# Optimization experiments

Hardware: AMD Instinct MI355X
Metric: run time of the kernel (lower is better)

Reference implementation:

```python
import jax, jax.numpy as jnp
import numpy as np

VARIANCE = 1.0  # prototorch euclidean_similarity default


def setup_inputs() -> dict:
    key = jax.random.key(0)
    k1, k2, k3 = jax.random.split(key, 3)
    B, D = 32768, 1024
    K, C = 5, 3  # sum([2,1,2]) components, len([2,1,2]) classes
    x = jax.random.normal(k1, (B, D), dtype=jnp.float32)
    components = jax.random.normal(k2, (K, D), dtype=jnp.float32)
    # PPRI: random probabilistic reasonings in [0,1], shape [K, C, 2]
    reasonings = jax.random.uniform(k3, (K, C, 2), dtype=jnp.float32)
    return {"x": x, "components": components, "reasonings": reasonings}


def reference(x, components, reasonings):
    # --- euclidean similarity: exp(-d(x, c)^2 / (2*variance)) ---
    # squared pairwise distances via expansion (avoids [B,K,D] intermediate)
    x2 = jnp.sum(x * x, axis=-1, keepdims=True)          # [B,1]
    c2 = jnp.sum(components * components, axis=-1)       # [K]
    d2 = x2 + c2[None, :] - 2.0 * (x @ components.T)     # [B,K]
    d2 = jnp.maximum(d2, 0.0)
    sims = jnp.exp(-d2 / (2.0 * VARIANCE))               # [B,K]

    # --- cbcc competition ---
    # reasonings [K,C,2] -> permute(2,1,0) -> [2,C,K], clamp to [0,1]
    R = jnp.clip(jnp.transpose(reasonings, (2, 1, 0)), 0.0, 1.0)
    A, Bneg = R[0], R[1]                                 # each [C,K]
    pk = A
    nk = (1.0 - A) * Bneg                                # [C,K]
    numerator = sims @ (pk - nk).T + jnp.sum(nk, axis=1) # [B,C]
    probs = numerator / jnp.sum(pk + nk, axis=1)         # [B,C]
    return probs
```

## Files before the change

kernel.cpp:

```cpp
#include <hip/hip_runtime.h>


#define DD 1024
#define KK 5
#define CC 3
#define F4_PER_ROW (DD / 4)
#define F4_PER_LANE (F4_PER_ROW / 64)

__global__ __launch_bounds__(256) void cbc_kernel(
    const float* __restrict__ x,
    const float* __restrict__ comps,
    const float* __restrict__ reas,
    float* __restrict__ out,
    int B)
{
    const int lane = threadIdx.x & 63;
    const int waves_per_block = blockDim.x >> 6;
    const int wave_global = blockIdx.x * waves_per_block + (threadIdx.x >> 6);
    const int n_waves = gridDim.x * waves_per_block;

    float4 cf[KK][F4_PER_LANE];
    const float4* comps4 = (const float4*)comps;
#pragma unroll
    for (int k = 0; k < KK; ++k)
#pragma unroll
        for (int j = 0; j < F4_PER_LANE; ++j)
            cf[k][j] = comps4[k * F4_PER_ROW + j * 64 + lane];

    float w[CC][KK], bias[CC], invden[CC];
#pragma unroll
    for (int c = 0; c < CC; ++c) {
        float nsum = 0.f, dsum = 0.f;
#pragma unroll
        for (int k = 0; k < KK; ++k) {
            float a = reas[k * (CC * 2) + c * 2 + 0];
            float b = reas[k * (CC * 2) + c * 2 + 1];
            a = fminf(fmaxf(a, 0.f), 1.f);
            b = fminf(fmaxf(b, 0.f), 1.f);
            float nk = (1.f - a) * b;
            w[c][k] = a - nk;
            nsum += nk;
            dsum += a + nk;
        }
        bias[c] = nsum;
        invden[c] = 1.f / dsum;
    }

    const float4* x4 = (const float4*)x;

    for (int row = wave_global; row < B; row += n_waves) {
        float acc[KK];
#pragma unroll
        for (int k = 0; k < KK; ++k) acc[k] = 0.f;

#pragma unroll
        for (int j = 0; j < F4_PER_LANE; ++j) {
            float4 xv = x4[(size_t)row * F4_PER_ROW + j * 64 + lane];
#pragma unroll
            for (int k = 0; k < KK; ++k) {
                float dx = xv.x - cf[k][j].x;
                float dy = xv.y - cf[k][j].y;
                float dz = xv.z - cf[k][j].z;
                float dw = xv.w - cf[k][j].w;
                acc[k] += dx * dx;
                acc[k] += dy * dy;
                acc[k] += dz * dz;
                acc[k] += dw * dw;
            }
        }

#pragma unroll
        for (int k = 0; k < KK; ++k) {
#pragma unroll
            for (int off = 32; off > 0; off >>= 1)
                acc[k] += __shfl_xor(acc[k], off, 64);
        }

        float sims[KK];
#pragma unroll
        for (int k = 0; k < KK; ++k)
            sims[k] = __expf(-0.5f * acc[k]);

        if (lane < CC) {
            const int c = lane;
            float num = bias[c];
#pragma unroll
            for (int k = 0; k < KK; ++k) num += sims[k] * w[c][k];
            out[(size_t)row * CC + c] = num * invden[c];
        }
    }
}

extern "C" void kernel_launch(void* const* d_in, const int* in_sizes, int n_in,
                              void* d_out, int out_size, void* d_ws, size_t ws_size,
                              hipStream_t stream) {
    const float* x = (const float*)d_in[0];
    const float* comps = (const float*)d_in[1];
    const float* reas = (const float*)d_in[2];
    float* out = (float*)d_out;
    const int B = in_sizes[0] / DD;

    const int blocks = 1024;
    cbc_kernel<<<blocks, 256, 0, stream>>>(x, comps, reas, out, B);
}
```

Baseline: 190.6 us.

## Stage components in LDS, process four rows per wave with register prefetch

Moves the component vectors from per-lane registers into shared memory and splits each wave into four 16-lane segments, each handling one row. The next row group is prefetched into registers while the current one is computed, and the distance is computed via the x²+c²−2x·c expansion with 16-lane shuffle reductions. The goal is to hide global-load latency and cut register pressure so two blocks can be resident. The cost is LDS read traffic and a larger prefetch register buffer.

New measurement: 198.9 us. 1.04x slower.

```diff
diff --git a/kernel.cpp b/kernel.cpp
--- a/kernel.cpp
+++ b/kernel.cpp
@@ -4,89 +4,140 @@
 #define DD 1024
 #define KK 5
 #define CC 3
-#define F4_PER_ROW (DD / 4)
-#define F4_PER_LANE (F4_PER_ROW / 64)
+#define F4R (DD / 4)
+#define JS 16
 
-__global__ __launch_bounds__(256) void cbc_kernel(
+__global__ __launch_bounds__(256, 2) void cbc_kernel(
     const float* __restrict__ x,
     const float* __restrict__ comps,
     const float* __restrict__ reas,
     float* __restrict__ out,
     int B)
 {
-    const int lane = threadIdx.x & 63;
+    __shared__ float4 cl[KK * F4R];
+
+    const int tid  = threadIdx.x;
+    const int lane = tid & 63;
+    const int seg  = lane >> 4;
+    const int t    = lane & 15;
+
     const int waves_per_block = blockDim.x >> 6;
-    const int wave_global = blockIdx.x * waves_per_block + (threadIdx.x >> 6);
+    const int wave    = blockIdx.x * waves_per_block + (tid >> 6);
     const int n_waves = gridDim.x * waves_per_block;
 
-    float4 cf[KK][F4_PER_LANE];
-    const float4* comps4 = (const float4*)comps;
+    const float4* c4 = (const float4*)comps;
+    for (int i = tid; i < KK * F4R; i += blockDim.x) cl[i] = c4[i];
+
+    const int c = (t < CC) ? t : 0;
+    float wv[KK], bias = 0.f, den = 0.f;
 #pragma unroll
-    for (int k = 0; k < KK; ++k)
-#pragma unroll
-        for (int j = 0; j < F4_PER_LANE; ++j)
-            cf[k][j] = comps4[k * F4_PER_ROW + j * 64 + lane];
+    for (int k = 0; k < KK; ++k) {
+        float a = reas[k * (CC * 2) + c * 2 + 0];
+        float b = reas[k * (CC * 2) + c * 2 + 1];
+        a = fminf(fmaxf(a, 0.f), 1.f);
+        b = fminf(fmaxf(b, 0.f), 1.f);
+        float nk = (1.f - a) * b;
+        wv[k] = a - nk;
+        bias += nk;
+        den  += a + nk;
+    }
+    const float invden = 1.f / den;
 
-    float w[CC][KK], bias[CC], invden[CC];
-#pragma unroll
-    for (int c = 0; c < CC; ++c) {
-        float nsum = 0.f, dsum = 0.f;
-#pragma unroll
-        for (int k = 0; k < KK; ++k) {
-            float a = reas[k * (CC * 2) + c * 2 + 0];
-            float b = reas[k * (CC * 2) + c * 2 + 1];
-            a = fminf(fmaxf(a, 0.f), 1.f);
-            b = fminf(fmaxf(b, 0.f), 1.f);
-            float nk = (1.f - a) * b;
-            w[c][k] = a - nk;
-            nsum += nk;
-            dsum += a + nk;
-        }
-        bias[c] = nsum;
-        invden[c] = 1.f / dsum;
-    }
+    __syncthreads();
 
     const float4* x4 = (const float4*)x;
+    const int ngroups = B >> 2;
 
-    for (int row = wave_global; row < B; row += n_waves) {
-        float acc[KK];
+    int g = wave;
+    if (g < ngroups) {
+        float4 xb[JS];
+        {
+            int row = g * 4 + seg; if (row >= B) row = B - 1;
+            const float4* p = x4 + (size_t)row * F4R + t;
 #pragma unroll
-        for (int k = 0; k < KK; ++k) acc[k] = 0.f;
+            for (int j = 0; j < JS; ++j) xb[j] = p[j * 16];
+        }
+
+        float c2[KK];
+#pragma unroll
+        for (int k = 0; k < KK; ++k) c2[k] = 0.f;
+#pragma unroll
+        for (int j = 0; j < JS; ++j) {
+#pragma unroll
+            for (int k = 0; k < KK; ++k) {
+                float4 cv = cl[k * F4R + j * 16 + t];
+                c2[k] += cv.x * cv.x; c2[k] += cv.y * cv.y;
+                c2[k] += cv.z * cv.z; c2[k] += cv.w * cv.w;
+            }
+        }
+#pragma unroll
+        for (int k = 0; k < KK; ++k)
+#pragma unroll
+            for (int off = 1; off < 16; off <<= 1)
+                c2[k] += __shfl_xor(c2[k], off, 64);
+
+        while (true) {
+            const int  gn = g + n_waves;
+            const bool hn = gn < ngroups;
+
+            float dot[KK], x2 = 0.f;
+#pragma unroll
+            for (int k = 0; k < KK; ++k) dot[k] = 0.f;
+
+            if (hn) {
+                int nrow = gn * 4 + seg; if (nrow >= B) nrow = B - 1;
+                const float4* np = x4 + (size_t)nrow * F4R + t;
+#pragma unroll
+                for (int j = 0; j < JS; ++j) {
+                    float4 xv = xb[j];
+                    xb[j] = np[j * 16];
+#pragma unroll
+                    for (int k = 0; k < KK; ++k) {
+                        float4 cv = cl[k * F4R + j * 16 + t];
+                        dot[k] += xv.x * cv.x; dot[k] += xv.y * cv.y;
+                        dot[k] += xv.z * cv.z; dot[k] += xv.w * cv.w;
+                    }
+                    x2 += xv.x * xv.x; x2 += xv.y * xv.y;
+                    x2 += xv.z * xv.z; x2 += xv.w * xv.w;
+                }
+            } else {
+#pragma unroll
+                for (int j = 0; j < JS; ++j) {
+                    float4 xv = xb[j];
+#pragma unroll
+                    for (int k = 0; k < KK; ++k) {
+                        float4 cv = cl[k * F4R + j * 16 + t];
+                        dot[k] += xv.x * cv.x; dot[k] += xv.y * cv.y;
+                        dot[k] += xv.z * cv.z; dot[k] += xv.w * cv.w;
+                    }
+                    x2 += xv.x * xv.x; x2 += xv.y * xv.y;
+                    x2 += xv.z * xv.z; x2 += xv.w * xv.w;
+                }
+            }
 
 #pragma unroll
-        for (int j = 0; j < F4_PER_LANE; ++j) {
-            float4 xv = x4[(size_t)row * F4_PER_ROW + j * 64 + lane];
+            for (int off = 1; off < 16; off <<= 1)
+                x2 += __shfl_xor(x2, off, 64);
 #pragma unroll
-            for (int k = 0; k < KK; ++k) {
-                float dx = xv.x - cf[k][j].x;
-                float dy = xv.y - cf[k][j].y;
-                float dz = xv.z - cf[k][j].z;
-                float dw = xv.w - cf[k][j].w;
-                acc[k] += dx * dx;
-                acc[k] += dy * dy;
-                acc[k] += dz * dz;
-                acc[k] += dw * dw;
+            for (int k = 0; k < KK; ++k)
+#pragma unroll
+                for (int off = 1; off < 16; off <<= 1)
+                    dot[k] += __shfl_xor(dot[k], off, 64);
+
+            const int row = g * 4 + seg;
+            if (t < CC && row < B) {
+                float num = bias;
+#pragma unroll
+                for (int k = 0; k < KK; ++k) {
+                    float d2 = x2 + c2[k] - 2.f * dot[k];
+                    d2 = fmaxf(d2, 0.f);
+                    num += __expf(-0.5f * d2) * wv[k];
+                }
+                out[(size_t)row * CC + t] = num * invden;
             }
-        }
 
-#pragma unroll
-        for (int k = 0; k < KK; ++k) {
-#pragma unroll
-            for (int off = 32; off > 0; off >>= 1)
-                acc[k] += __shfl_xor(acc[k], off, 64);
-        }
-
-        float sims[KK];
-#pragma unroll
-        for (int k = 0; k < KK; ++k)
-            sims[k] = __expf(-0.5f * acc[k]);
-
-        if (lane < CC) {
-            const int c = lane;
-            float num = bias[c];
-#pragma unroll
-            for (int k = 0; k < KK; ++k) num += sims[k] * w[c][k];
-            out[(size_t)row * CC + c] = num * invden[c];
+            if (!hn) break;
+            g = gn;
         }
     }
 }
@@ -98,8 +149,11 @@
     const float* comps = (const float*)d_in[1];
     const float* reas = (const float*)d_in[2];
     float* out = (float*)d_out;
-    const int B = in_sizes[0] / DD;
+    const int B = in_sizes[0] / (DD * 4);
+
+    const int Brows = in_sizes[0] / DD;
 
     const int blocks = 1024;
-    cbc_kernel<<<blocks, 256, 0, stream>>>(x, comps, reas, out, B);
+    cbc_kernel<<<blocks, 256, 0, stream>>>(x, comps, reas, out, Brows);
+    (void)B;
 }
```

## Stage components in LDS, batch row loads, raise occupancy and grid

Applied to the files above, without the earlier changes.

Moves the component vectors from per-lane registers into shared memory, which frees registers, and sets launch bounds to 8 blocks per SM to raise occupancy. All four float4 loads of a row are issued up front to increase memory-level parallelism. The per-class weights are now computed once per lane instead of as a 3x5 table, and the grid is doubled. The trade-off is extra LDS reads for every row, plus a block-wide load and barrier at kernel start.

After: 269.9 us. 1.42x slower.

```diff
diff --git a/kernel.cpp b/kernel.cpp
--- a/kernel.cpp
+++ b/kernel.cpp
@@ -4,64 +4,65 @@
 #define DD 1024
 #define KK 5
 #define CC 3
-#define F4_PER_ROW (DD / 4)
-#define F4_PER_LANE (F4_PER_ROW / 64)
+#define F4R (DD / 4)
+#define JN (F4R / 64)
 
-__global__ __launch_bounds__(256) void cbc_kernel(
+__global__ __launch_bounds__(256, 8) void cbc_kernel(
     const float* __restrict__ x,
     const float* __restrict__ comps,
     const float* __restrict__ reas,
     float* __restrict__ out,
     int B)
 {
-    const int lane = threadIdx.x & 63;
+    __shared__ float4 cl[KK * F4R];
+
+    const int tid  = threadIdx.x;
+    const int lane = tid & 63;
     const int waves_per_block = blockDim.x >> 6;
-    const int wave_global = blockIdx.x * waves_per_block + (threadIdx.x >> 6);
+    const int wave    = blockIdx.x * waves_per_block + (tid >> 6);
     const int n_waves = gridDim.x * waves_per_block;
 
-    float4 cf[KK][F4_PER_LANE];
-    const float4* comps4 = (const float4*)comps;
+    const float4* c4 = (const float4*)comps;
+    for (int i = tid; i < KK * F4R; i += blockDim.x) cl[i] = c4[i];
+
+    const int c = (lane < CC) ? lane : 0;
+    float wv[KK], bias = 0.f, den = 0.f;
 #pragma unroll
-    for (int k = 0; k < KK; ++k)
-#pragma unroll
-        for (int j = 0; j < F4_PER_LANE; ++j)
-            cf[k][j] = comps4[k * F4_PER_ROW + j * 64 + lane];
+    for (int k = 0; k < KK; ++k) {
+        float a = reas[k * (CC * 2) + c * 2 + 0];
+        float b = reas[k * (CC * 2) + c * 2 + 1];
+        a = fminf(fmaxf(a, 0.f), 1.f);
+        b = fminf(fmaxf(b, 0.f), 1.f);
+        float nk = (1.f - a) * b;
+        wv[k] = a - nk;
+        bias += nk;
+        den  += a + nk;
+    }
+    const float invden = 1.f / den;
 
-    float w[CC][KK], bias[CC], invden[CC];
-#pragma unroll
-    for (int c = 0; c < CC; ++c) {
-        float nsum = 0.f, dsum = 0.f;
-#pragma unroll
-        for (int k = 0; k < KK; ++k) {
-            float a = reas[k * (CC * 2) + c * 2 + 0];
-            float b = reas[k * (CC * 2) + c * 2 + 1];
-            a = fminf(fmaxf(a, 0.f), 1.f);
-            b = fminf(fmaxf(b, 0.f), 1.f);
-            float nk = (1.f - a) * b;
-            w[c][k] = a - nk;
-            nsum += nk;
-            dsum += a + nk;
-        }
-        bias[c] = nsum;
-        invden[c] = 1.f / dsum;
-    }
+    __syncthreads();
 
     const float4* x4 = (const float4*)x;
 
-    for (int row = wave_global; row < B; row += n_waves) {
+    for (int row = wave; row < B; row += n_waves) {
+        float4 xv[JN];
+        const float4* p = x4 + (size_t)row * F4R + lane;
+#pragma unroll
+        for (int j = 0; j < JN; ++j) xv[j] = p[j * 64];
+
         float acc[KK];
 #pragma unroll
         for (int k = 0; k < KK; ++k) acc[k] = 0.f;
 
 #pragma unroll
-        for (int j = 0; j < F4_PER_LANE; ++j) {
-            float4 xv = x4[(size_t)row * F4_PER_ROW + j * 64 + lane];
+        for (int j = 0; j < JN; ++j) {
 #pragma unroll
             for (int k = 0; k < KK; ++k) {
-                float dx = xv.x - cf[k][j].x;
-                float dy = xv.y - cf[k][j].y;
-                float dz = xv.z - cf[k][j].z;
-                float dw = xv.w - cf[k][j].w;
+                float4 cv = cl[k * F4R + j * 64 + lane];
+                float dx = xv[j].x - cv.x;
+                float dy = xv[j].y - cv.y;
+                float dz = xv[j].z - cv.z;
+                float dw = xv[j].w - cv.w;
                 acc[k] += dx * dx;
                 acc[k] += dy * dy;
                 acc[k] += dz * dz;
@@ -76,17 +77,12 @@
                 acc[k] += __shfl_xor(acc[k], off, 64);
         }
 
-        float sims[KK];
+        if (lane < CC) {
+            float num = bias;
 #pragma unroll
-        for (int k = 0; k < KK; ++k)
-            sims[k] = __expf(-0.5f * acc[k]);
-
-        if (lane < CC) {
-            const int c = lane;
-            float num = bias[c];
-#pragma unroll
-            for (int k = 0; k < KK; ++k) num += sims[k] * w[c][k];
-            out[(size_t)row * CC + c] = num * invden[c];
+            for (int k = 0; k < KK; ++k)
+                num += __expf(-0.5f * acc[k]) * wv[k];
+            out[(size_t)row * CC + lane] = num * invden;
         }
     }
 }
@@ -100,6 +96,6 @@
     float* out = (float*)d_out;
     const int B = in_sizes[0] / DD;
 
-    const int blocks = 1024;
+    const int blocks = 2048;
     cbc_kernel<<<blocks, 256, 0, stream>>>(x, comps, reas, out, B);
 }
```
